# Kernel tuning notes

Hardware: AMD Instinct MI355X
Metric: run time of the kernel (lower is better)

## Reference

```python
import jax, jax.numpy as jnp
import numpy as np


def setup_inputs() -> dict:
    key = jax.random.key(0)
    k1, k2, k3 = jax.random.split(key, 3)
    B, Cin, H, W = 64, 16, 256, 256
    Cout, K = 64, 3
    x = jax.random.normal(k1, (B, Cin, H, W), dtype=jnp.float32)
    # PyTorch Conv2d init: uniform(-s, s) with s = 1/sqrt(Cin*K*K)
    s = 1.0 / np.sqrt(Cin * K * K)
    conv_weight = jax.random.uniform(k2, (Cout, Cin, K, K), dtype=jnp.float32, minval=-s, maxval=s)
    conv_bias = jax.random.uniform(k3, (Cout,), dtype=jnp.float32, minval=-s, maxval=s)
    return {"x": x, "conv_weight": conv_weight, "conv_bias": conv_bias}


def reference(x, conv_weight, conv_bias):
    # conv2d (stride 1, no padding) -> min over channels -> tanh -> tanh
    y = jax.lax.conv_general_dilated(
        x, conv_weight,
        window_strides=(1, 1), padding='VALID',
        dimension_numbers=('NCHW', 'OIHW', 'NCHW'))
    y = y + conv_bias[None, :, None, None]          # [B, Cout, H', W']
    y = jnp.min(y, axis=1, keepdims=True)           # [B, 1, H', W']
    return jnp.tanh(jnp.tanh(y))
```

## Files before the change

### kernel.cpp

```cpp
#include <hip/hip_runtime.h>

typedef _Float16 f16x8 __attribute__((ext_vector_type(8)));
typedef _Float16 f16x2 __attribute__((ext_vector_type(2)));
typedef float    f32x4 __attribute__((ext_vector_type(4)));

#define CIN    16
#define COUT   64
#define H      256
#define W      256
#define OH     254
#define OW     254
#define TH     32
#define TW     32
#define IN_H   (TH + 2)
#define IN_W   (TW + 2)
#define IN_PIX (IN_H * IN_W)
#define NU     (IN_H * 8 * 9)

__device__ __forceinline__ float ftanh(float x) {
  float e = __expf(x + x);
  float r = __builtin_amdgcn_rcpf(e + 1.0f);
  return 1.0f - (r + r);
}

__device__ __forceinline__ f32x4 vmin4(f32x4 a, f32x4 b) {
  f32x4 r;
  r[0] = fminf(a[0], b[0]); r[1] = fminf(a[1], b[1]);
  r[2] = fminf(a[2], b[2]); r[3] = fminf(a[3], b[3]);
  return r;
}

__global__ __launch_bounds__(256, 1)
void weight_prep(const float* __restrict__ wgt, _Float16* __restrict__ ws) {
  const int t = threadIdx.x;
  uint32_t* wz = (uint32_t*)(ws + 9 * COUT * 16);
  wz[t] = 0u; wz[t + 256] = 0u;
  const f32x4* w4 = (const f32x4*)wgt;
#pragma unroll
  for (int k = 0; k < 9; ++k) {
    const f32x4 v = w4[9 * t + k];
#pragma unroll
    for (int e = 0; e < 4; ++e) {
      const int g   = (9 * t + k) * 4 + e;
      const int co  = g / 144;
      const int r   = g - 144 * co;
      const int ci  = r / 9;
      const int tap = r - 9 * ci;
      ws[(tap * COUT + co) * 16 + ci] = (_Float16)v[e];
    }
  }
}

__global__ __launch_bounds__(256, 4)
void conv_min_tanh_mfma(const float* __restrict__ x, const _Float16* __restrict__ ws,
                        const float* __restrict__ bias, float* __restrict__ out) {
  __shared__ __align__(16) _Float16 xs[IN_PIX * CIN];

  const int t   = threadIdx.x;
  const int b   = blockIdx.z;
  const int ow0 = blockIdx.x * TW;
  const int oh0 = blockIdx.y * TH;

  const int lane = t & 63;
  const int ln   = lane & 15;
  const int q    = lane >> 4;
  const int qh   = q >> 1;
  const int ql   = q & 1;

  f16x8 wf[5][4];
#pragma unroll
  for (int s = 0; s < 5; ++s) {
    const int tap = 2 * s + qh;
#pragma unroll
    for (int mt = 0; mt < 4; ++mt) {
      const int cout = mt * 16 + ln;
      wf[s][mt] = *(const f16x8*)(ws + (tap * COUT + cout) * 16 + ql * 8);
    }
  }

  {
    f32x4 sv0[2], sv1[2];
    int   sbase[2], sj[2];
    bool  sact[2];

    auto prep = [&](int i, int slot) {
      const int  u   = t + 256 * i;
      const bool act = (u < NU);
      const int  s   = u / 9;
      const int  j   = u - 9 * s;
      const int  row = s >> 3;
      const int  cp  = s & 7;
      const int  ih  = oh0 + row;
      const int  iw0 = ow0 + 4 * j;
      const f32x4 z = {0.f, 0.f, 0.f, 0.f};
      sv0[slot] = z; sv1[slot] = z;
      if (act && ih < H && iw0 + 3 < W) {
        const float* p = x + (((size_t)b * CIN + 2 * cp) * H + ih) * W + iw0;
        sv0[slot] = *(const f32x4*)p;
        sv1[slot] = *(const f32x4*)(p + H * W);
      }
      sbase[slot] = (row * IN_W + 4 * j) * CIN + 2 * cp;
      sj[slot]    = j;
      sact[slot]  = act;
    };
    auto flush = [&](int slot) {
      if (sact[slot]) {
        const int base = sbase[slot];
        const int j    = sj[slot];
#pragma unroll
        for (int e = 0; e < 4; ++e) {
          if (4 * j + e < IN_W) {
            f16x2 h;
            h[0] = (_Float16)sv0[slot][e];
            h[1] = (_Float16)sv1[slot][e];
            *(f16x2*)(&xs[base + e * CIN]) = h;
          }
        }
      }
    };

    prep(0, 0);
#pragma unroll
    for (int i = 0; i < 10; ++i) {
      if (i < 9) prep(i + 1, (i + 1) & 1);
      flush(i & 1);
    }
  }

  int xoff[5];
#pragma unroll
  for (int s = 0; s < 5; ++s) {
    int tap = 2 * s + qh;
    if (tap > 8) tap = 8;
    const int kh = tap / 3;
    const int kw = tap - kh * 3;
    xoff[s] = (kh * IN_W + kw) * CIN + ql * 8;
  }

  f32x4 binit[4];
#pragma unroll
  for (int mt = 0; mt < 4; ++mt)
#pragma unroll
    for (int r = 0; r < 4; ++r)
      binit[mt][r] = bias[mt * 16 + q * 4 + r];

  __syncthreads();

  const int wv = t >> 6;
  for (int rr = 0; rr < 8; ++rr) {
    const int row = wv * 8 + rr;
#pragma unroll
    for (int ct = 0; ct < 2; ++ct) {
      const int base_idx = (row * IN_W + ct * 16 + ln) * CIN;
      f32x4 a0 = binit[0], a1 = binit[1], a2 = binit[2], a3 = binit[3];
#pragma unroll
      for (int s = 0; s < 5; ++s) {
        f16x8 xf = *(const f16x8*)(&xs[base_idx + xoff[s]]);
        a0 = __builtin_amdgcn_mfma_f32_16x16x32_f16(wf[s][0], xf, a0, 0, 0, 0);
        a1 = __builtin_amdgcn_mfma_f32_16x16x32_f16(wf[s][1], xf, a1, 0, 0, 0);
        a2 = __builtin_amdgcn_mfma_f32_16x16x32_f16(wf[s][2], xf, a2, 0, 0, 0);
        a3 = __builtin_amdgcn_mfma_f32_16x16x32_f16(wf[s][3], xf, a3, 0, 0, 0);
      }
      f32x4 m4 = vmin4(vmin4(a0, a1), vmin4(a2, a3));
      float v = fminf(fminf(m4[0], m4[1]), fminf(m4[2], m4[3]));
      v = fminf(v, __shfl_xor(v, 16));
      v = fminf(v, __shfl_xor(v, 32));
      v = ftanh(ftanh(v));
      const int oh = oh0 + row;
      const int ow = ow0 + ct * 16 + ln;
      if (q == 0 && oh < OH && ow < OW)
        out[((size_t)b * OH + oh) * OW + ow] = v;
    }
  }
}

extern "C" void kernel_launch(void* const* d_in, const int* in_sizes, int n_in,
                              void* d_out, int out_size, void* d_ws, size_t ws_size,
                              hipStream_t stream) {
  const float* x    = (const float*)d_in[0];
  const float* wgt  = (const float*)d_in[1];
  const float* bias = (const float*)d_in[2];
  float* out = (float*)d_out;
  _Float16* ws = (_Float16*)d_ws;

  weight_prep<<<dim3(1, 1, 1), 256, 0, stream>>>(wgt, ws);
  dim3 grid((OW + TW - 1) / TW, (OH + TH - 1) / TH, 64);
  conv_min_tanh_mfma<<<grid, 256, 0, stream>>>(x, ws, bias, out);
}
```

Baseline: 411.7 us.

## Split input staging so half the waves compute while others load remaining rows

```diff
diff --git a/kernel.cpp b/kernel.cpp
--- a/kernel.cpp
+++ b/kernel.cpp
@@ -15,7 +15,8 @@
 #define IN_H   (TH + 2)
 #define IN_W   (TW + 2)
 #define IN_PIX (IN_H * IN_W)
-#define NU     (IN_H * 8 * 9)
+#define U_LOW  (18 * 8 * 9)
+#define U_ALL  (IN_H * 8 * 9)
 
 __device__ __forceinline__ float ftanh(float x) {
   float e = __expf(x + x);
@@ -31,10 +32,13 @@
 }
 
 __global__ __launch_bounds__(256, 1)
-void weight_prep(const float* __restrict__ wgt, _Float16* __restrict__ ws) {
+void weight_prep(const float* __restrict__ wgt, const float* __restrict__ bias,
+                 _Float16* __restrict__ ws) {
   const int t = threadIdx.x;
   uint32_t* wz = (uint32_t*)(ws + 9 * COUT * 16);
   wz[t] = 0u; wz[t + 256] = 0u;
+  __syncthreads();
+  if (t < COUT) ws[(9 * COUT + t) * 16] = (_Float16)bias[t];
   const f32x4* w4 = (const f32x4*)wgt;
 #pragma unroll
   for (int k = 0; k < 9; ++k) {
@@ -53,7 +57,7 @@
 
 __global__ __launch_bounds__(256, 4)
 void conv_min_tanh_mfma(const float* __restrict__ x, const _Float16* __restrict__ ws,
-                        const float* __restrict__ bias, float* __restrict__ out) {
+                        float* __restrict__ out) {
   __shared__ __align__(16) _Float16 xs[IN_PIX * CIN];
 
   const int t   = threadIdx.x;
@@ -66,6 +70,7 @@
   const int q    = lane >> 4;
   const int qh   = q >> 1;
   const int ql   = q & 1;
+  const int wv   = t >> 6;
 
   f16x8 wf[5][4];
 #pragma unroll
@@ -78,54 +83,8 @@
     }
   }
 
-  {
-    f32x4 sv0[2], sv1[2];
-    int   sbase[2], sj[2];
-    bool  sact[2];
-
-    auto prep = [&](int i, int slot) {
-      const int  u   = t + 256 * i;
-      const bool act = (u < NU);
-      const int  s   = u / 9;
-      const int  j   = u - 9 * s;
-      const int  row = s >> 3;
-      const int  cp  = s & 7;
-      const int  ih  = oh0 + row;
-      const int  iw0 = ow0 + 4 * j;
-      const f32x4 z = {0.f, 0.f, 0.f, 0.f};
-      sv0[slot] = z; sv1[slot] = z;
-      if (act && ih < H && iw0 + 3 < W) {
-        const float* p = x + (((size_t)b * CIN + 2 * cp) * H + ih) * W + iw0;
-        sv0[slot] = *(const f32x4*)p;
-        sv1[slot] = *(const f32x4*)(p + H * W);
-      }
-      sbase[slot] = (row * IN_W + 4 * j) * CIN + 2 * cp;
-      sj[slot]    = j;
-      sact[slot]  = act;
-    };
-    auto flush = [&](int slot) {
-      if (sact[slot]) {
-        const int base = sbase[slot];
-        const int j    = sj[slot];
-#pragma unroll
-        for (int e = 0; e < 4; ++e) {
-          if (4 * j + e < IN_W) {
-            f16x2 h;
-            h[0] = (_Float16)sv0[slot][e];
-            h[1] = (_Float16)sv1[slot][e];
-            *(f16x2*)(&xs[base + e * CIN]) = h;
-          }
-        }
-      }
-    };
-
-    prep(0, 0);
-#pragma unroll
-    for (int i = 0; i < 10; ++i) {
-      if (i < 9) prep(i + 1, (i + 1) & 1);
-      flush(i & 1);
-    }
-  }
+  f16x8 cst = {};
+  if (q == 2) cst[0] = (_Float16)1.0f;
 
   int xoff[5];
 #pragma unroll
@@ -137,41 +96,97 @@
     xoff[s] = (kh * IN_W + kw) * CIN + ql * 8;
   }
 
-  f32x4 binit[4];
-#pragma unroll
-  for (int mt = 0; mt < 4; ++mt)
-#pragma unroll
-    for (int r = 0; r < 4; ++r)
-      binit[mt][r] = bias[mt * 16 + q * 4 + r];
-
+  f32x4 sv0[2], sv1[2];
+  int   sbase[2], sj[2];
+  bool  sact[2];
+
+  auto prep = [&](int u, int uend, int slot) {
+    const bool act = (u < uend);
+    const int  s   = u / 9;
+    const int  j   = u - 9 * s;
+    const int  row = s >> 3;
+    const int  cp  = s & 7;
+    const int  ih  = oh0 + row;
+    const int  iw0 = ow0 + 4 * j;
+    const f32x4 z = {0.f, 0.f, 0.f, 0.f};
+    sv0[slot] = z; sv1[slot] = z;
+    if (act && ih < H && iw0 + 3 < W) {
+      const float* p = x + (((size_t)b * CIN + 2 * cp) * H + ih) * W + iw0;
+      sv0[slot] = *(const f32x4*)p;
+      sv1[slot] = *(const f32x4*)(p + H * W);
+    }
+    sbase[slot] = (row * IN_W + 4 * j) * CIN + 2 * cp;
+    sj[slot]    = j;
+    sact[slot]  = act;
+  };
+  auto flush = [&](int slot) {
+    if (sact[slot]) {
+      const int base = sbase[slot];
+      const int j    = sj[slot];
+#pragma unroll
+      for (int e = 0; e < 4; ++e) {
+        if (4 * j + e < IN_W) {
+          f16x2 h;
+          h[0] = (_Float16)sv0[slot][e];
+          h[1] = (_Float16)sv1[slot][e];
+          *(f16x2*)(&xs[base + e * CIN]) = h;
+        }
+      }
+    }
+  };
+
+  auto compute8 = [&]() {
+    for (int rr = 0; rr < 8; ++rr) {
+      const int row = wv * 8 + rr;
+#pragma unroll
+      for (int ct = 0; ct < 2; ++ct) {
+        const int base_idx = (row * IN_W + ct * 16 + ln) * CIN;
+        f32x4 a0 = {}, a1 = {}, a2 = {}, a3 = {};
+#pragma unroll
+        for (int s = 0; s < 5; ++s) {
+          f16x8 xf;
+          if (s == 4 && qh == 1) xf = cst;
+          else xf = *(const f16x8*)(&xs[base_idx + xoff[s]]);
+          a0 = __builtin_amdgcn_mfma_f32_16x16x32_f16(wf[s][0], xf, a0, 0, 0, 0);
+          a1 = __builtin_amdgcn_mfma_f32_16x16x32_f16(wf[s][1], xf, a1, 0, 0, 0);
+          a2 = __builtin_amdgcn_mfma_f32_16x16x32_f16(wf[s][2], xf, a2, 0, 0, 0);
+          a3 = __builtin_amdgcn_mfma_f32_16x16x32_f16(wf[s][3], xf, a3, 0, 0, 0);
+        }
+        f32x4 m4 = vmin4(vmin4(a0, a1), vmin4(a2, a3));
+        float v = fminf(fminf(m4[0], m4[1]), fminf(m4[2], m4[3]));
+        v = fminf(v, __shfl_xor(v, 16));
+        v = fminf(v, __shfl_xor(v, 32));
+        v = ftanh(ftanh(v));
+        const int oh = oh0 + row;
+        const int ow = ow0 + ct * 16 + ln;
+        if (q == 0 && oh < OH && ow < OW)
+          out[((size_t)b * OH + oh) * OW + ow] = v;
+      }
+    }
+  };
+
+  prep(t, U_LOW, 0);
+#pragma unroll
+  for (int i = 0; i < 6; ++i) {
+    if (i < 5) prep(t + 256 * (i + 1), U_LOW, (i + 1) & 1);
+    flush(i & 1);
+  }
   __syncthreads();
 
-  const int wv = t >> 6;
-  for (int rr = 0; rr < 8; ++rr) {
-    const int row = wv * 8 + rr;
-#pragma unroll
-    for (int ct = 0; ct < 2; ++ct) {
-      const int base_idx = (row * IN_W + ct * 16 + ln) * CIN;
-      f32x4 a0 = binit[0], a1 = binit[1], a2 = binit[2], a3 = binit[3];
-#pragma unroll
-      for (int s = 0; s < 5; ++s) {
-        f16x8 xf = *(const f16x8*)(&xs[base_idx + xoff[s]]);
-        a0 = __builtin_amdgcn_mfma_f32_16x16x32_f16(wf[s][0], xf, a0, 0, 0, 0);
-        a1 = __builtin_amdgcn_mfma_f32_16x16x32_f16(wf[s][1], xf, a1, 0, 0, 0);
-        a2 = __builtin_amdgcn_mfma_f32_16x16x32_f16(wf[s][2], xf, a2, 0, 0, 0);
-        a3 = __builtin_amdgcn_mfma_f32_16x16x32_f16(wf[s][3], xf, a3, 0, 0, 0);
-      }
-      f32x4 m4 = vmin4(vmin4(a0, a1), vmin4(a2, a3));
-      float v = fminf(fminf(m4[0], m4[1]), fminf(m4[2], m4[3]));
-      v = fminf(v, __shfl_xor(v, 16));
-      v = fminf(v, __shfl_xor(v, 32));
-      v = ftanh(ftanh(v));
-      const int oh = oh0 + row;
-      const int ow = ow0 + ct * 16 + ln;
-      if (q == 0 && oh < OH && ow < OW)
-        out[((size_t)b * OH + oh) * OW + ow] = v;
-    }
-  }
+  if (wv < 2) {
+    compute8();
+  } else {
+    const int tb = t - 128;
+    prep(U_LOW + tb, U_ALL, 0);
+#pragma unroll
+    for (int i = 0; i < 9; ++i) {
+      if (i < 8) prep(U_LOW + tb + 128 * (i + 1), U_ALL, (i + 1) & 1);
+      flush(i & 1);
+    }
+  }
+  __syncthreads();
+
+  if (wv >= 2) compute8();
 }
 
 extern "C" void kernel_launch(void* const* d_in, const int* in_sizes, int n_in,
@@ -183,7 +198,7 @@
   float* out = (float*)d_out;
   _Float16* ws = (_Float16*)d_ws;
 
-  weight_prep<<<dim3(1, 1, 1), 256, 0, stream>>>(wgt, ws);
+  weight_prep<<<dim3(1, 1, 1), 256, 0, stream>>>(wgt, bias, ws);
   dim3 grid((OW + TW - 1) / TW, (OH + TH - 1) / TH, 64);
-  conv_min_tanh_mfma<<<grid, 256, 0, stream>>>(x, ws, bias, out);
-}
+  conv_min_tanh_mfma<<<grid, 256, 0, stream>>>(x, ws, out);
+}
```

Result: slower. 455.2 us (+10.6%).
